# Optimization experiments

Measured on AMD Instinct MI355X. Metric: run time of the kernel, lower is better.

The kernel has to match this reference:

```python
import jax, jax.numpy as jnp
import numpy as np

B, S, D, H = 2, 2048, 768, 12
HD = D // H


def setup_inputs() -> dict:
    key = jax.random.key(0)
    ks = jax.random.split(key, 6)
    x = jax.random.normal(ks[0], (B, S, D), dtype=jnp.float32)
    # causal mask: 1.0 where attention is disallowed (upper triangle), broadcast to [B,H,S,S]
    mask = (1.0 - jnp.tril(jnp.ones((S, S), dtype=jnp.float32)))[None, None]
    std = 0.02
    Wq = jax.random.normal(ks[1], (D, D), dtype=jnp.float32) * std
    Wk = jax.random.normal(ks[2], (D, D), dtype=jnp.float32) * std
    Wv = jax.random.normal(ks[3], (D, D), dtype=jnp.float32) * std
    Wo = jax.random.normal(ks[4], (D, D), dtype=jnp.float32) * (1.0 / np.sqrt(D))
    bq = jnp.zeros((D,), jnp.float32)
    bk = jnp.zeros((D,), jnp.float32)
    bv = jnp.zeros((D,), jnp.float32)
    bo = jnp.zeros((D,), jnp.float32)
    return {"x": x, "mask": mask, "Wq": Wq, "bq": bq, "Wk": Wk, "bk": bk,
            "Wv": Wv, "bv": bv, "Wo": Wo, "bo": bo}


def _split_heads(t):
    # [B,S,D] -> [B,H,S,hd]
    return t.reshape(B, S, H, HD).transpose(0, 2, 1, 3)


def reference(x, mask, Wq, bq, Wk, bk, Wv, bv, Wo, bo):
    q = _split_heads(x @ Wq + bq)
    k = _split_heads(x @ Wk + bk)
    v = _split_heads(x @ Wv + bv)
    scale = 1.0 / jnp.sqrt(jnp.asarray(HD, x.dtype))
    logits = jnp.einsum('bhqd,bhkd->bhqk', q, k) * scale  # [B,H,S,S]
    logits = logits + mask * (-1e9)
    attn = jax.nn.softmax(logits, axis=-1)
    ctx = jnp.einsum('bhqk,bhkd->bhqd', attn, v)          # [B,H,S,hd]
    ctx = ctx.transpose(0, 2, 1, 3).reshape(B, S, D)
    return ctx @ Wo + bo
```

## Files before the change

### kernel.cpp

```cpp
#include <hip/hip_runtime.h>
#include <math.h>

typedef unsigned short u16;
typedef unsigned int u32;
typedef unsigned long long u64;
typedef short bf16x8 __attribute__((ext_vector_type(8)));
typedef float f32x4 __attribute__((ext_vector_type(4)));
typedef float f32x16 __attribute__((ext_vector_type(16)));
typedef u32 u32x4 __attribute__((ext_vector_type(4)));

#define MFMA(a, b, c) __builtin_amdgcn_mfma_f32_16x16x32_bf16((a), (b), (c), 0, 0, 0)
#define MFMA32(a, b, c) __builtin_amdgcn_mfma_f32_32x32x16_bf16((a), (b), (c), 0, 0, 0)

#define BB 2
#define SS 2048
#define DD 768
#define HH 12
#define MROWS (BB * SS)
#define SCL 0.1803368801111244f


#if defined(__has_builtin)
#if __has_builtin(__builtin_amdgcn_global_load_lds)
#define HAS_GLL 1
#endif
#if __has_builtin(__builtin_amdgcn_exp2f)
#define HAS_EXP2 1
#endif
#endif
#ifndef HAS_GLL
#define HAS_GLL 0
#endif
#ifndef HAS_EXP2
#define HAS_EXP2 0
#endif

__device__ __forceinline__ float fexp2(float x) {
#if HAS_EXP2
  return __builtin_amdgcn_exp2f(x);
#else
  return exp2f(x);
#endif
}

__device__ __forceinline__ u16 f2bf(float f) {
  u32 u = __float_as_uint(f);
  u += 0x7FFFu + ((u >> 16) & 1u);
  return (u16)(u >> 16);
}
__device__ __forceinline__ float bf2f(u16 v) {
  return __uint_as_float(((u32)v) << 16);
}
__device__ __forceinline__ u32 cvtpk(float a, float b) {
  u32 r;
  asm("v_cvt_pk_bf16_f32 %0, %1, %2" : "=v"(r) : "v"(a), "v"(b));
  return r;
}

#if HAS_GLL
__device__ __forceinline__ void gload_lds16(const u16* g, u16* l) {
  __builtin_amdgcn_global_load_lds(
      (const __attribute__((address_space(1))) void*)(u64)(uintptr_t)g,
      (__attribute__((address_space(3))) void*)(u64)(uintptr_t)l, 16, 0, 0);
}
#endif

__global__ __launch_bounds__(256) void k_convert(const float* __restrict__ in,
                                                 u16* __restrict__ out, int n) {
  int i = (blockIdx.x * 256 + threadIdx.x) * 4;
  if (i < n) {
    float4 v = *(const float4*)(in + i);
    ushort4 o;
    o.x = f2bf(v.x); o.y = f2bf(v.y); o.z = f2bf(v.z); o.w = f2bf(v.w);
    *(ushort4*)(out + i) = o;
  }
}

__global__ __launch_bounds__(256) void k_transpose_w(
    const float* __restrict__ Wq, const float* __restrict__ Wk,
    const float* __restrict__ Wv, const float* __restrict__ Wo,
    u16* __restrict__ out) {
  const float* W = (blockIdx.z == 0) ? Wq : (blockIdx.z == 1) ? Wk
                   : (blockIdx.z == 2) ? Wv : Wo;
  u16* o = out + (size_t)blockIdx.z * DD * DD;
  __shared__ float tile[32][33];
  int kt = blockIdx.x * 32, nt = blockIdx.y * 32;
  int tx = threadIdx.x & 31, ty = threadIdx.x >> 5;
#pragma unroll
  for (int r = 0; r < 4; r++) {
    int row = ty + r * 8;
    tile[row][tx] = W[(size_t)(kt + row) * DD + nt + tx];
  }
  __syncthreads();
#pragma unroll
  for (int r = 0; r < 4; r++) {
    int row = ty + r * 8;
    o[(size_t)(nt + row) * DD + kt + tx] = f2bf(tile[tx][row]);
  }
}

template <bool OUT_BF16>
__device__ __forceinline__ void gemm128(const u16* __restrict__ A,
                                        const u16* __restrict__ Bt,
                                        const float* __restrict__ bias,
                                        void* __restrict__ Cout, int m0, int n0) {
  __shared__ __align__(16) u16 Al[128 * 32];
  __shared__ __align__(16) u16 Bl[128 * 32];
  int t = threadIdx.x;
  int lane = t & 63, w = t >> 6;
  int wm = (w >> 1) * 64, wn = (w & 1) * 64;
  int l15 = lane & 15, l4 = lane >> 4;
  f32x4 acc[4][4];
#pragma unroll
  for (int i = 0; i < 4; i++)
#pragma unroll
    for (int j = 0; j < 4; j++) acc[i][j] = (f32x4){0.f, 0.f, 0.f, 0.f};

#if HAS_GLL
  int srow = w * 32 + (lane >> 2);
  int skc = (lane & 3) * 8;
#endif

  for (int k0 = 0; k0 < DD; k0 += 32) {
#if HAS_GLL
#pragma unroll
    for (int rep = 0; rep < 2; rep++) {
      int row = srow + rep * 16;
      gload_lds16(A + (size_t)(m0 + row) * DD + k0 + skc,
                  &Al[(w * 32 + rep * 16) * 32]);
      gload_lds16(Bt + (size_t)(n0 + row) * DD + k0 + skc,
                  &Bl[(w * 32 + rep * 16) * 32]);
    }
#else
#pragma unroll
    for (int rep = 0; rep < 2; rep++) {
      int idx = rep * 256 + t;
      int row = idx >> 2, kc = (idx & 3) * 8;
      *(uint4*)&Al[row * 32 + kc] =
          *(const uint4*)(A + (size_t)(m0 + row) * DD + k0 + kc);
      *(uint4*)&Bl[row * 32 + kc] =
          *(const uint4*)(Bt + (size_t)(n0 + row) * DD + k0 + kc);
    }
#endif
    __syncthreads();
    bf16x8 af[4], bfr[4];
#pragma unroll
    for (int mb = 0; mb < 4; mb++)
      af[mb] = *(const bf16x8*)(&Al[(wm + mb * 16 + l15) * 32 + l4 * 8]);
#pragma unroll
    for (int nb = 0; nb < 4; nb++)
      bfr[nb] = *(const bf16x8*)(&Bl[(wn + nb * 16 + l15) * 32 + l4 * 8]);
#pragma unroll
    for (int mb = 0; mb < 4; mb++)
#pragma unroll
      for (int nb = 0; nb < 4; nb++)
        acc[mb][nb] = MFMA(af[mb], bfr[nb], acc[mb][nb]);
    __syncthreads();
  }
#pragma unroll
  for (int nb = 0; nb < 4; nb++) {
    int col = n0 + wn + nb * 16 + l15;
    float bs = bias[col];
#pragma unroll
    for (int mb = 0; mb < 4; mb++) {
#pragma unroll
      for (int r = 0; r < 4; r++) {
        int row = m0 + wm + mb * 16 + l4 * 4 + r;
        float vv = acc[mb][nb][r] + bs;
        if (OUT_BF16)
          ((u16*)Cout)[(size_t)row * DD + col] = f2bf(vv);
        else
          ((float*)Cout)[(size_t)row * DD + col] = vv;
      }
    }
  }
}

__global__ __launch_bounds__(256) void k_gemm_qkv(
    const u16* __restrict__ xb, const u16* __restrict__ Wt,
    const float* __restrict__ bq, const float* __restrict__ bk,
    const float* __restrict__ bv, u16* __restrict__ qkv) {
  int z = blockIdx.z;
  const u16* Bt = Wt + (size_t)z * DD * DD;
  const float* bias = (z == 0) ? bq : (z == 1) ? bk : bv;
  u16* out = qkv + (size_t)z * MROWS * DD;
  gemm128<true>(xb, Bt, bias, out, blockIdx.x * 128, blockIdx.y * 128);
}

__global__ __launch_bounds__(256) void k_gemm_out(
    const u16* __restrict__ ctx, const u16* __restrict__ Wot,
    const float* __restrict__ bo, float* __restrict__ out) {
  gemm128<false>(ctx, Wot, bo, out, blockIdx.x * 128, blockIdx.y * 128);
}

__global__ __launch_bounds__(256) void k_attn2(
    const u16* __restrict__ qb, const u16* __restrict__ kb,
    const u16* __restrict__ vb, u16* __restrict__ PO,
    float* __restrict__ PM, float* __restrict__ PL, u16* __restrict__ ctx,
    int CH2, int tot) {
  __shared__ __align__(16) u16 Vt[2][64 * 32];
  int bh = blockIdx.x;
  int s = tot - 1 - (int)blockIdx.y;
  int qt = 15, pre = 0;
#pragma unroll 16
  for (int q = 0; q < 16; q++) {
    int nq = (4 * (q + 1) + CH2 - 1) / CH2;
    if (s < pre + nq) { qt = q; break; }
    pre += nq;
  }
  int c = s - pre;
  int ntile = 4 * (qt + 1);
  int n = (ntile + CH2 - 1) / CH2;
  int len = (ntile - 1 - c) / n + 1;

  int b = bh / HH, h = bh % HH;
  int t = threadIdx.x, wq = t >> 6, lane = t & 63;
  int l31 = lane & 31, hi = lane >> 5;
  size_t rowbase = (size_t)b * SS;
  int hcol = h * 64;
  int qtq = qt * 128 + wq * 32;

  const u16* qp = qb + (rowbase + qtq + l31) * DD + hcol + hi * 8;
  bf16x8 qf0 = *(const bf16x8*)(qp);
  bf16x8 qf1 = *(const bf16x8*)(qp + 16);
  bf16x8 qf2 = *(const bf16x8*)(qp + 32);
  bf16x8 qf3 = *(const bf16x8*)(qp + 48);

  const u16* kbase = kb + rowbase * DD + hcol;
  const u16* vbase = vb + rowbase * DD + hcol;

  f32x16 o0, o1;
#pragma unroll
  for (int r = 0; r < 16; r++) { o0[r] = 0.f; o1[r] = 0.f; }
  float m_r = -3e38f, l_r = 0.f;

  int vk = t & 31, vd0 = (t >> 5) * 8;
  {
    uint4 v0 = *(const uint4*)(vbase + (size_t)(c * 32 + vk) * DD + vd0);
    u16 el[8];
    *(uint4*)el = v0;
    char* Vn = (char*)Vt[0];
#pragma unroll
    for (int ii = 0; ii < 8; ii++) {
      int d = vd0 + ii;
      *(u16*)(Vn + ((d * 64 + vk * 2) ^ (((d >> 1) & 3) << 4))) = el[ii];
    }
  }
  int dsw = ((l31 >> 1) & 3) << 4;

  for (int i = 0; i < len; i++) {
    int k32 = c + i * n;
    __syncthreads();
    uint4 vnext;
    if (i + 1 < len) {
      int nk = c + (i + 1) * n;
      vnext = *(const uint4*)(vbase + (size_t)(nk * 32 + vk) * DD + vd0);
    }
    bool act = (k32 * 32 <= qtq + 31);
    if (act) {
      const u16* kp = kbase + (size_t)(k32 * 32 + l31) * DD + hi * 8;
      bf16x8 kf0 = *(const bf16x8*)(kp);
      bf16x8 kf1 = *(const bf16x8*)(kp + 16);
      bf16x8 kf2 = *(const bf16x8*)(kp + 32);
      bf16x8 kf3 = *(const bf16x8*)(kp + 48);
      f32x16 sa;
#pragma unroll
      for (int r = 0; r < 16; r++) sa[r] = 0.f;
      __builtin_amdgcn_s_setprio(1);
      sa = MFMA32(kf0, qf0, sa);
      sa = MFMA32(kf1, qf1, sa);
      sa = MFMA32(kf2, qf2, sa);
      sa = MFMA32(kf3, qf3, sa);
      __builtin_amdgcn_s_setprio(0);
      float p[16];
#pragma unroll
      for (int r = 0; r < 16; r++) p[r] = sa[r] * SCL;
      if (k32 * 32 + 31 > qtq) {
        int qg = qtq + l31;
#pragma unroll
        for (int r = 0; r < 16; r++) {
          int kg = k32 * 32 + (r & 3) + 8 * (r >> 2) + 4 * hi;
          p[r] = (kg > qg) ? -1e30f : p[r];
        }
      }
      float mx = p[0];
#pragma unroll
      for (int r = 1; r < 16; r++) mx = fmaxf(mx, p[r]);
      mx = fmaxf(mx, __shfl_xor(mx, 32, 64));
      float mn = fmaxf(m_r, mx);
      float al = fexp2(m_r - mn);
      m_r = mn;
      float rs = 0.f;
#pragma unroll
      for (int r = 0; r < 16; r++) {
        p[r] = fexp2(p[r] - mn);
        rs += p[r];
      }
      rs += __shfl_xor(rs, 32, 64);
      l_r = l_r * al + rs;
      u32 cc0 = cvtpk(p[0], p[1]), cc1 = cvtpk(p[2], p[3]);
      u32 cc2 = cvtpk(p[4], p[5]), cc3 = cvtpk(p[6], p[7]);
      u32 cc4 = cvtpk(p[8], p[9]), cc5 = cvtpk(p[10], p[11]);
      u32 cc6 = cvtpk(p[12], p[13]), cc7 = cvtpk(p[14], p[15]);
      u32 xx0 = __shfl_xor(cc0, 32, 64), xx1 = __shfl_xor(cc1, 32, 64);
      u32 xx2 = __shfl_xor(cc2, 32, 64), xx3 = __shfl_xor(cc3, 32, 64);
      u32 xx4 = __shfl_xor(cc4, 32, 64), xx5 = __shfl_xor(cc5, 32, 64);
      u32 xx6 = __shfl_xor(cc6, 32, 64), xx7 = __shfl_xor(cc7, 32, 64);
      u32x4 P0 = {hi ? xx2 : cc0, hi ? xx3 : cc1, hi ? cc2 : xx0, hi ? cc3 : xx1};
      u32x4 P1 = {hi ? xx6 : cc4, hi ? xx7 : cc5, hi ? cc6 : xx4, hi ? cc7 : xx5};
      bf16x8 pb0 = __builtin_bit_cast(bf16x8, P0);
      bf16x8 pb1 = __builtin_bit_cast(bf16x8, P1);
#pragma unroll
      for (int r = 0; r < 16; r++) { o0[r] *= al; o1[r] *= al; }
      const char* Vc = (const char*)Vt[i & 1];
      bf16x8 a00 = *(const bf16x8*)(Vc + ((l31 * 64 + hi * 16) ^ dsw));
      bf16x8 a01 = *(const bf16x8*)(Vc + ((l31 * 64 + 32 + hi * 16) ^ dsw));
      bf16x8 a10 = *(const bf16x8*)(Vc + (((32 + l31) * 64 + hi * 16) ^ dsw));
      bf16x8 a11 = *(const bf16x8*)(Vc + (((32 + l31) * 64 + 32 + hi * 16) ^ dsw));
      __builtin_amdgcn_s_setprio(1);
      o0 = MFMA32(a00, pb0, o0);
      o0 = MFMA32(a01, pb1, o0);
      o1 = MFMA32(a10, pb0, o1);
      o1 = MFMA32(a11, pb1, o1);
      __builtin_amdgcn_s_setprio(0);
    }
    if (i + 1 < len) {
      u16 el[8];
      *(uint4*)el = vnext;
      char* Vn = (char*)Vt[(i + 1) & 1];
#pragma unroll
      for (int ii = 0; ii < 8; ii++) {
        int d = vd0 + ii;
        *(u16*)(Vn + ((d * 64 + vk * 2) ^ (((d >> 1) & 3) << 4))) = el[ii];
      }
    }
  }
  float inv = 1.f / l_r;
  ushort4 g[8];
#pragma unroll
  for (int rq = 0; rq < 4; rq++) {
    g[rq].x = f2bf(o0[rq * 4 + 0] * inv);
    g[rq].y = f2bf(o0[rq * 4 + 1] * inv);
    g[rq].z = f2bf(o0[rq * 4 + 2] * inv);
    g[rq].w = f2bf(o0[rq * 4 + 3] * inv);
    g[4 + rq].x = f2bf(o1[rq * 4 + 0] * inv);
    g[4 + rq].y = f2bf(o1[rq * 4 + 1] * inv);
    g[4 + rq].z = f2bf(o1[rq * 4 + 2] * inv);
    g[4 + rq].w = f2bf(o1[rq * 4 + 3] * inv);
  }
  if (n == 1) {
    u16* dst = ctx + (rowbase + qtq + l31) * DD + hcol;
#pragma unroll
    for (int db = 0; db < 2; db++)
#pragma unroll
      for (int rq = 0; rq < 4; rq++)
        *(ushort4*)(dst + db * 32 + rq * 8 + hi * 4) = g[db * 4 + rq];
  } else {
    size_t gs = (size_t)bh * tot + pre + c;
    u16* po = PO + gs * 8192 + (size_t)(wq * 32 + l31) * 64;
#pragma unroll
    for (int db = 0; db < 2; db++)
#pragma unroll
      for (int rq = 0; rq < 4; rq++)
        *(ushort4*)(po + db * 32 + rq * 8 + hi * 4) = g[db * 4 + rq];
    if (hi == 0) {
      PM[gs * 128 + wq * 32 + l31] = m_r;
      PL[gs * 128 + wq * 32 + l31] = l_r;
    }
  }
}

__global__ __launch_bounds__(256) void k_combine2(
    const u16* __restrict__ PO, const float* __restrict__ PM,
    const float* __restrict__ PL, u16* __restrict__ ctx, int CH2, int tot,
    int qt0) {
  int bh = blockIdx.x, qt = qt0 + blockIdx.y;
  int b = bh / HH, h = bh % HH;
  int ntile = 4 * (qt + 1);
  int n = (ntile + CH2 - 1) / CH2;
  int pre = 0;
#pragma unroll 16
  for (int q = 0; q < 16; q++)
    if (q < qt) pre += (4 * (q + 1) + CH2 - 1) / CH2;
  size_t base = (size_t)bh * tot + pre;
  int t = threadIdx.x;
  int ql = t >> 1, d0 = (t & 1) * 32;
  float w[8];
  float M = -3e38f;
#pragma unroll 8
  for (int i = 0; i < 8; i++) {
    if (i < n) {
      float mi = PM[(base + i) * 128 + ql];
      w[i] = mi;
      M = fmaxf(M, mi);
    }
  }
  float L = 0.f;
#pragma unroll 8
  for (int i = 0; i < 8; i++) {
    if (i < n) {
      float wi = PL[(base + i) * 128 + ql] * fexp2(w[i] - M);
      w[i] = wi;
      L += wi;
    }
  }
  float inv = 1.f / L;
  float acc[32];
#pragma unroll
  for (int j = 0; j < 32; j++) acc[j] = 0.f;
#pragma unroll 8
  for (int i = 0; i < 8; i++) {
    if (i < n) {
      float wi = w[i] * inv;
      const u16* p = PO + (base + i) * 8192 + (size_t)ql * 64 + d0;
#pragma unroll
      for (int q8 = 0; q8 < 4; q8++) {
        bf16x8 v = *(const bf16x8*)(p + q8 * 8);
#pragma unroll
        for (int j = 0; j < 8; j++) acc[q8 * 8 + j] += wi * bf2f((u16)v[j]);
      }
    }
  }
  u16 ob[32];
#pragma unroll
  for (int j = 0; j < 32; j++) ob[j] = f2bf(acc[j]);
  u16* dst = ctx + ((size_t)b * SS + qt * 128 + ql) * DD + h * 64 + d0;
#pragma unroll
  for (int q8 = 0; q8 < 4; q8++)
    *(uint4*)(dst + q8 * 8) = *(uint4*)(ob + q8 * 8);
}

extern "C" void kernel_launch(void* const* d_in, const int* in_sizes, int n_in,
                              void* d_out, int out_size, void* d_ws, size_t ws_size,
                              hipStream_t stream) {
  const float* x  = (const float*)d_in[0];
  const float* Wq = (const float*)d_in[2];
  const float* bq = (const float*)d_in[3];
  const float* Wk = (const float*)d_in[4];
  const float* bk = (const float*)d_in[5];
  const float* Wv = (const float*)d_in[6];
  const float* bv = (const float*)d_in[7];
  const float* Wo = (const float*)d_in[8];
  const float* bo = (const float*)d_in[9];
  float* out = (float*)d_out;

  char* ws = (char*)d_ws;
  const size_t XN = (size_t)MROWS * DD;
  const size_t WN = (size_t)DD * DD;
  u16* xb  = (u16*)ws;
  u16* Wt  = (u16*)(ws + XN * 2);
  u16* qkv = (u16*)(ws + XN * 2 + WN * 8);
  u16* ctx = (u16*)(ws + XN * 2 + WN * 8 + XN * 6);
  const size_t base = XN * 2 + WN * 8 + XN * 6 + XN * 2;

  int CH2 = 64, tot = 0;
  {
    const int cands[4] = {8, 16, 32, 64};
    for (int ci = 0; ci < 4; ci++) {
      int ch = cands[ci];
      int tt = 0;
      for (int q = 0; q < 16; q++) tt += (4 * (q + 1) + ch - 1) / ch;
      size_t need = base + (size_t)24 * tt * 8192 * 2 +
                    2 * (size_t)24 * tt * 128 * 4;
      if (ws_size >= need) { CH2 = ch; tot = tt; break; }
      if (ci == 3) { CH2 = ch; tot = tt; }
    }
  }
  const size_t NCHUNK = (size_t)24 * tot;
  u16*   PO = (u16*)(ws + base);
  float* PM = (float*)(ws + base + NCHUNK * 8192 * 2);
  float* PL = PM + NCHUNK * 128;
  int qt0 = CH2 / 4;

  k_convert<<<dim3((int)(XN / 1024)), 256, 0, stream>>>(x, xb, (int)XN);
  k_transpose_w<<<dim3(24, 24, 4), 256, 0, stream>>>(Wq, Wk, Wv, Wo, Wt);
  k_gemm_qkv<<<dim3(32, 6, 3), 256, 0, stream>>>(xb, Wt, bq, bk, bv, qkv);
  k_attn2<<<dim3(24, tot), 256, 0, stream>>>(qkv, qkv + XN, qkv + 2 * XN, PO, PM,
                                             PL, ctx, CH2, tot);
  if (qt0 < 16)
    k_combine2<<<dim3(24, 16 - qt0), 256, 0, stream>>>(PO, PM, PL, ctx, CH2, tot,
                                                       qt0);
  k_gemm_out<<<dim3(32, 6), 256, 0, stream>>>(ctx, Wt + 3 * WN, bo, out);
}
```

Measured before the change: 121.5 us.

## Stage K tiles in double-buffered LDS shared across waves in attention

In the split attention kernel, K fragments are no longer read from global memory by each of the four waves. Wave 0 now prefetches the next 32-row K tile into a double-buffered LDS array (through global_load_lds where available), and all waves read their MFMA operands from LDS. The aim is to cut redundant global K traffic across waves and to overlap the K load with the current iteration's compute. In exchange it uses more LDS, and correctness depends on the existing __syncthreads ordering the async LDS writes against the reads.

Measured after the change: 110.2 us. 1.1x faster.

```diff
diff --git a/kernel.cpp b/kernel.cpp
--- a/kernel.cpp
+++ b/kernel.cpp
@@ -199,6 +199,7 @@
     float* __restrict__ PM, float* __restrict__ PL, u16* __restrict__ ctx,
     int CH2, int tot) {
   __shared__ __align__(16) u16 Vt[2][64 * 32];
+  __shared__ __align__(16) u16 Kl[2][2048];
   int bh = blockIdx.x;
   int s = tot - 1 - (int)blockIdx.y;
   int qt = 15, pre = 0;
@@ -246,11 +247,38 @@
       *(u16*)(Vn + ((d * 64 + vk * 2) ^ (((d >> 1) & 3) << 4))) = el[ii];
     }
   }
+#if HAS_GLL
+  if (wq == 0) {
+    const u16* kp = kbase + (size_t)(c * 32 + l31) * DD + hi * 8;
+#pragma unroll
+    for (int j = 0; j < 4; j++) gload_lds16(kp + j * 16, &Kl[0][j * 512]);
+  }
+#else
+  if (wq == 0) {
+    const u16* kp = kbase + (size_t)(c * 32 + l31) * DD + hi * 8;
+#pragma unroll
+    for (int j = 0; j < 4; j++)
+      *(uint4*)&Kl[0][j * 512 + lane * 8] = *(const uint4*)(kp + j * 16);
+  }
+#endif
   int dsw = ((l31 >> 1) & 3) << 4;
 
   for (int i = 0; i < len; i++) {
     int k32 = c + i * n;
     __syncthreads();
+    if (wq == 0 && i + 1 < len) {
+      int nk = c + (i + 1) * n;
+      const u16* kp = kbase + (size_t)(nk * 32 + l31) * DD + hi * 8;
+#if HAS_GLL
+#pragma unroll
+      for (int j = 0; j < 4; j++)
+        gload_lds16(kp + j * 16, &Kl[(i + 1) & 1][j * 512]);
+#else
+#pragma unroll
+      for (int j = 0; j < 4; j++)
+        *(uint4*)&Kl[(i + 1) & 1][j * 512 + lane * 8] = *(const uint4*)(kp + j * 16);
+#endif
+    }
     uint4 vnext;
     if (i + 1 < len) {
       int nk = c + (i + 1) * n;
@@ -258,11 +286,11 @@
     }
     bool act = (k32 * 32 <= qtq + 31);
     if (act) {
-      const u16* kp = kbase + (size_t)(k32 * 32 + l31) * DD + hi * 8;
-      bf16x8 kf0 = *(const bf16x8*)(kp);
-      bf16x8 kf1 = *(const bf16x8*)(kp + 16);
-      bf16x8 kf2 = *(const bf16x8*)(kp + 32);
-      bf16x8 kf3 = *(const bf16x8*)(kp + 48);
+      const char* Kc = (const char*)Kl[i & 1];
+      bf16x8 kf0 = *(const bf16x8*)(Kc + lane * 16);
+      bf16x8 kf1 = *(const bf16x8*)(Kc + 1024 + lane * 16);
+      bf16x8 kf2 = *(const bf16x8*)(Kc + 2048 + lane * 16);
+      bf16x8 kf3 = *(const bf16x8*)(Kc + 3072 + lane * 16);
       f32x16 sa;
 #pragma unroll
       for (int r = 0; r < 16; r++) sa[r] = 0.f;
```
